# Kernel optimization log

Measured on AMD Instinct MI355X. Metric: run time of the kernel, lower is better.

## Reference

```python
import jax, jax.numpy as jnp
import numpy as np

# Neuron / sim params from init_kwargs
THETA = 1.0        # thr
TAU_RHO = 0.5      # grad_width (surrogate width, used only in backward)
SCALE_RHO = 1.0    # grad_scale
NUM_TS = 100


def avg_pool4(x):
    # SLAYER pool(4): conv3d with constant weight 1/16 over 4x4 spatial, stride 4 == average pool
    N, C, H, W, T = x.shape
    return x.reshape(N, C, H // 4, 4, W // 4, 4, T).mean(axis=(3, 5))


def conv7(x, w):
    # torch Conv3d over (H, W, T) with kernel (7,7,1), padding (3,3,0), stride 1, no bias
    return jax.lax.conv_general_dilated(
        x, w, window_strides=(1, 1, 1),
        padding=((3, 3), (3, 3), (0, 0)),
        dimension_numbers=('NCHWT', 'OIHWT', 'NCHWT'))


def psp(x):
    # IAF synaptic kernel = Heaviside step => psp is cumulative sum over time (Ts = 1)
    return jnp.cumsum(x, axis=-1)


def spike_scan(p):
    # Integrate-and-fire spike generation with reset-by-subtraction (scaleRef=1):
    # v[t] = psp[t] - theta * (#spikes before t); spike when v[t] >= theta.
    p_t = jnp.moveaxis(p, -1, 0)  # [T, N, C, H, W]
    count0 = jnp.zeros(p.shape[:-1], p.dtype)

    def step(count, pt):
        v = pt - THETA * count
        s = (v >= THETA).astype(pt.dtype)
        return count + s, (s, v)

    _, (s, v) = jax.lax.scan(step, count0, p_t)
    return jnp.moveaxis(s, 0, -1), jnp.moveaxis(v, 0, -1)


def setup_inputs() -> dict:
    key = jax.random.key(0)
    k0, k1, k2, k3 = jax.random.split(key, 4)
    data = jax.random.uniform(k0, (8, 2, 256, 256, NUM_TS), dtype=jnp.float32)
    # learned parameters (bias=False in SLAYER conv/dense)
    w_conv0 = jax.random.normal(k1, (4, 2, 7, 7, 1), dtype=jnp.float32) * 0.2
    w_conv1 = jax.random.normal(k2, (8, 4, 7, 7, 1), dtype=jnp.float32) * 0.2
    w_dense = jax.random.normal(k3, (2, 8, 4, 4, 1), dtype=jnp.float32) * 0.2
    return {"data": data, "w_conv0": w_conv0, "w_conv1": w_conv1, "w_dense": w_dense}


def reference(data, w_conv0, w_conv1, w_dense):
    x = conv7(avg_pool4(data), w_conv0)     # [8,4,64,64,T]
    s0, _ = spike_scan(psp(x))
    x = conv7(avg_pool4(s0), w_conv1)       # [8,8,16,16,T]
    s1, _ = spike_scan(psp(x))
    x = avg_pool4(s1)                       # [8,8,4,4,T]
    # dense((4,4,8) -> 2): conv3d whose kernel spans the full spatial extent
    out = jnp.einsum('nchwt,ochw->not', x, w_dense[..., 0])  # [8,2,T]
    return out
```

## Files before the change

### kernel.cpp

```cpp
#include <hip/hip_runtime.h>
#include <hip/hip_bf16.h>
#include <stdint.h>


#define T_ 100

__global__ __launch_bounds__(256) void k1_pool0(const float* __restrict__ in,
                                                double* __restrict__ out) {
    __shared__ double lds[64 * 101];
    int b = blockIdx.x;
    int h = b & 63, c = (b >> 6) & 1, n = b >> 7;
    const float* inb = in + ((size_t)((n * 2 + c) * 256 + 4 * h) * 256) * 100;
    for (int k = 0; k < 7; ++k) {
        int e = threadIdx.x + (k << 8);
        if (e < 1600) {
            int w = e / 25, tq = e % 25;
            double s0 = 0.0, s1 = 0.0, s2 = 0.0, s3 = 0.0;
            #pragma unroll
            for (int a = 0; a < 4; ++a) {
                #pragma unroll
                for (int bb = 0; bb < 4; ++bb) {
                    const float4 v = *reinterpret_cast<const float4*>(
                        &inb[((size_t)(a * 256 + 4 * w + bb)) * 100 + 4 * tq]);
                    s0 += (double)v.x;
                    s1 += (double)v.y;
                    s2 += (double)v.z;
                    s3 += (double)v.w;
                }
            }
            double* lp = &lds[w * 101 + 4 * tq];
            lp[0] = s0 * 0.0625;
            lp[1] = s1 * 0.0625;
            lp[2] = s2 * 0.0625;
            lp[3] = s3 * 0.0625;
        }
    }
    __syncthreads();
    double* outb = out + ((size_t)(n * 2 + c) * 100) * 4096 + h * 64;
    for (int k = 0; k < 25; ++k) {
        int oi = threadIdx.x + (k << 8);
        int t = oi >> 6, w = oi & 63;
        outb[(size_t)t * 4096 + w] = lds[w * 101 + t];
    }
}

__global__ __launch_bounds__(256, 2) void k2a_conv0(const double* __restrict__ pooled0,
                                                    const float* __restrict__ wc0,
                                                    double* __restrict__ x0) {
    __shared__ double tile[2 * 22 * 70];
    __shared__ double wlds[392];
    int b = blockIdx.x;
    int hs = b & 3;
    int t = (b >> 2) % 100;
    int n = b / 400;
    int tid = threadIdx.x;

    for (int i = tid; i < 392; i += 256) wlds[i] = (double)wc0[i];
    {
        int lane = tid & 63, wv = tid >> 6;
        for (int r = wv; r < 44; r += 4) {
            int ci = (r >= 22) ? 1 : 0;
            int row = r - ci * 22;
            int habs = hs * 16 + row - 3;
            const double* src =
                &pooled0[((size_t)((n * 2 + ci) * 100 + t)) * 4096 + habs * 64];
            double* dst = &tile[(ci * 22 + row) * 70];
            int wabs = lane - 3;
            bool hok = (unsigned)habs < 64u;
            dst[lane] = (hok && (unsigned)wabs < 64u) ? src[wabs] : 0.0;
            if (lane < 6) {
                int wabs2 = lane + 61;
                dst[lane + 64] = (hok && (unsigned)wabs2 < 64u) ? src[wabs2] : 0.0;
            }
        }
    }
    __syncthreads();

    int w = tid & 63, hq = tid >> 6;
    int hl0 = hq * 4;
    double acc[4][4];
    #pragma unroll
    for (int co = 0; co < 4; ++co)
        #pragma unroll
        for (int j = 0; j < 4; ++j) acc[co][j] = 0.0;

    for (int ci = 0; ci < 2; ++ci) {
        #pragma unroll
        for (int kh = 0; kh < 7; ++kh) {
            const double* wp = &wlds[ci * 49 + kh * 7];
            #pragma unroll
            for (int j = 0; j < 4; ++j) {
                const double* r = &tile[(ci * 22 + hl0 + kh + j) * 70 + w];
                double v0 = r[0], v1 = r[1], v2 = r[2], v3 = r[3];
                double v4 = r[4], v5 = r[5], v6 = r[6];
                #pragma unroll
                for (int co = 0; co < 4; ++co) {
                    acc[co][j] += v0 * wp[co * 98 + 0];
                    acc[co][j] += v1 * wp[co * 98 + 1];
                    acc[co][j] += v2 * wp[co * 98 + 2];
                    acc[co][j] += v3 * wp[co * 98 + 3];
                    acc[co][j] += v4 * wp[co * 98 + 4];
                    acc[co][j] += v5 * wp[co * 98 + 5];
                    acc[co][j] += v6 * wp[co * 98 + 6];
                }
            }
        }
    }
    #pragma unroll
    for (int co = 0; co < 4; ++co)
        #pragma unroll
        for (int j = 0; j < 4; ++j)
            x0[(((size_t)(n * 4 + co) * 64 + (hs * 16 + hl0 + j)) * 100 + t) * 64 + w] =
                acc[co][j];
}

__global__ __launch_bounds__(256) void k2b_scan0_pool(const double* __restrict__ x0,
                                                      float* __restrict__ pooled1) {
    __shared__ uint8_t lsp[10][256];
    int bid = blockIdx.x;
    int g = bid >> 4, hp = bid & 15;
    int tid = threadIdx.x;
    int r = tid >> 6, w = tid & 63;
    size_t base = ((size_t)(g * 64 + hp * 4 + r) * 100) * 64 + w;
    double p = 0.0;
    int cnt = 0;
    for (int tc = 0; tc < 10; ++tc) {
        double v[10];
        #pragma unroll
        for (int j = 0; j < 10; ++j)
            v[j] = x0[base + (size_t)(tc * 10 + j) * 64];
        #pragma unroll
        for (int j = 0; j < 10; ++j) {
            p += v[j];
            int sp = (p - (double)cnt) >= 1.0;
            cnt += sp;
            lsp[j][tid] = (uint8_t)sp;
        }
        __syncthreads();
        if (tid < 160) {
            int t = tid >> 4, wp = tid & 15;
            int isum = 0;
            #pragma unroll
            for (int rr = 0; rr < 4; ++rr) {
                uint32_t u = *reinterpret_cast<const uint32_t*>(&lsp[t][rr * 64 + 4 * wp]);
                isum += (int)(u & 0xffu) + (int)((u >> 8) & 0xffu) +
                        (int)((u >> 16) & 0xffu) + (int)(u >> 24);
            }
            pooled1[((size_t)g * 100 + tc * 10 + t) * 256 + hp * 16 + wp] =
                (float)isum * 0.0625f;
        }
        __syncthreads();
    }
}

#define TC2 5
__global__ __launch_bounds__(128) void k2_conv0_scan(const double* __restrict__ pooled0,
                                                     const float* __restrict__ wc0,
                                                     uint8_t* __restrict__ s0) {
    __shared__ double tile[2 * 7 * TC2 * 70];
    int b = blockIdx.x;
    int h = b & 63, n = b >> 6;
    int tid = threadIdx.x;
    int w = tid & 63, cog = tid >> 6;
    int co0 = 2 * cog, co1 = co0 + 1;
    for (int i = tid; i < 2 * 7 * TC2 * 70; i += 128) tile[i] = 0.0;
    double p0 = 0.0, p1 = 0.0;
    int c0 = 0, c1 = 0;
    for (int ch = 0; ch < T_ / TC2; ++ch) {
        int t0 = ch * TC2;
        __syncthreads();
        for (int k = 0; k < 35; ++k) {
            int e = tid + (k << 7);
            int ww = e & 63, rowid = e >> 6;
            int ci = rowid / 35, rem = rowid % 35;
            int tt = rem / 7, r = rem % 7;
            int habs = h - 3 + r;
            if ((unsigned)habs < 64u)
                tile[((ci * 7 + r) * TC2 + tt) * 70 + ww + 3] =
                    pooled0[((size_t)((n * 2 + ci) * 100 + t0 + tt)) * 4096 + habs * 64 + ww];
        }
        __syncthreads();
        double acc0[TC2], acc1[TC2];
        #pragma unroll
        for (int tt = 0; tt < TC2; ++tt) { acc0[tt] = 0.0; acc1[tt] = 0.0; }
        for (int ci = 0; ci < 2; ++ci) {
            for (int kh = 0; kh < 7; ++kh) {
                const double* trow = &tile[((ci * 7 + kh) * TC2) * 70];
                const float* wr0 = &wc0[co0 * 98 + ci * 49 + kh * 7];
                const float* wr1 = &wc0[co1 * 98 + ci * 49 + kh * 7];
                #pragma unroll
                for (int kw = 0; kw < 7; ++kw) {
                    double wa = (double)wr0[kw];
                    double wb = (double)wr1[kw];
                    #pragma unroll
                    for (int tt = 0; tt < TC2; ++tt) {
                        double v = trow[tt * 70 + w + kw];
                        acc0[tt] += v * wa;
                        acc1[tt] += v * wb;
                    }
                }
            }
        }
        #pragma unroll
        for (int tt = 0; tt < TC2; ++tt) {
            size_t ob = ((size_t)((n * 4 + co0) * 100 + t0 + tt)) * 4096 + h * 64 + w;
            p0 += acc0[tt];
            int sp0 = (p0 - (double)c0) >= 1.0;
            c0 += sp0;
            s0[ob] = (uint8_t)sp0;
            size_t ob1 = ((size_t)((n * 4 + co1) * 100 + t0 + tt)) * 4096 + h * 64 + w;
            p1 += acc1[tt];
            int sp1 = (p1 - (double)c1) >= 1.0;
            c1 += sp1;
            s0[ob1] = (uint8_t)sp1;
        }
    }
}

__global__ __launch_bounds__(256) void k3_pool1(const uint8_t* __restrict__ s0,
                                                float* __restrict__ pooled1) {
    int oi = blockIdx.x * 256 + threadIdx.x;
    int w = oi & 15, h = (oi >> 4) & 15;
    int tc = oi >> 8;
    int t = tc % 100, nc = tc / 100;
    const uint8_t* base = s0 + ((size_t)nc * 100 + t) * 4096;
    int isum = 0;
    #pragma unroll
    for (int a = 0; a < 4; ++a) {
        uint32_t v = *reinterpret_cast<const uint32_t*>(&base[(4 * h + a) * 64 + 4 * w]);
        isum += (int)(v & 0xffu) + (int)((v >> 8) & 0xffu) +
                (int)((v >> 16) & 0xffu) + (int)(v >> 24);
    }
    pooled1[oi] = (float)isum * 0.0625f;
}

__global__ __launch_bounds__(256) void k4a_conv1(const float* __restrict__ pooled1,
                                                 const float* __restrict__ wc1,
                                                 double* __restrict__ x1) {
    __shared__ float tile[4 * 22 * 24];
    __shared__ float wl[1568];
    int b = blockIdx.x;
    int n = b / 100, t = b % 100;
    int tid = threadIdx.x;
    for (int i = tid; i < 4 * 22 * 24; i += 256) tile[i] = 0.0f;
    for (int i = tid; i < 1568; i += 256) wl[i] = wc1[i];
    __syncthreads();
    for (int k = 0; k < 4; ++k) {
        int e = tid + (k << 8);
        int w = e & 15, rowid = e >> 4;
        int ci = rowid >> 4, hr3 = rowid & 15;
        tile[(ci * 22 + hr3 + 3) * 24 + 3 + w] =
            pooled1[((size_t)((n * 4 + ci) * 100 + t)) * 256 + hr3 * 16 + w];
    }
    __syncthreads();
    int h = tid >> 4, w = tid & 15;
    double acc[8];
    #pragma unroll
    for (int co = 0; co < 8; ++co) acc[co] = 0.0;
    for (int ci = 0; ci < 4; ++ci) {
        for (int kh = 0; kh < 7; ++kh) {
            const float* trow = &tile[(ci * 22 + h + kh) * 24];
            const float* wr = &wl[ci * 49 + kh * 7];
            #pragma unroll
            for (int kw = 0; kw < 7; ++kw) {
                double v = (double)trow[w + kw];
                #pragma unroll
                for (int co = 0; co < 8; ++co)
                    acc[co] += v * (double)wr[co * 196 + kw];
            }
        }
    }
    #pragma unroll
    for (int co = 0; co < 8; ++co)
        x1[(((size_t)(n * 8 + co) * 4 + (tid >> 6)) * 100 + t) * 64 + (tid & 63)] =
            acc[co];
}

__global__ __launch_bounds__(64) void k4b_scan1(const double* __restrict__ x1,
                                                uint8_t* __restrict__ s1) {
    int bid = blockIdx.x;
    int g8 = bid >> 2, q = bid & 3;
    size_t rbase = ((size_t)(g8 * 4 + q) * 100) * 64 + threadIdx.x;
    size_t wbase = (size_t)g8 * 100 * 256 + (q << 6) + threadIdx.x;
    double p = 0.0;
    int cnt = 0;
    for (int tc = 0; tc < 10; ++tc) {
        double v[10];
        #pragma unroll
        for (int j = 0; j < 10; ++j)
            v[j] = x1[rbase + (size_t)(tc * 10 + j) * 64];
        #pragma unroll
        for (int j = 0; j < 10; ++j) {
            p += v[j];
            int sp = (p - (double)cnt) >= 1.0;
            cnt += sp;
            s1[wbase + (size_t)(tc * 10 + j) * 256] = (uint8_t)sp;
        }
    }
}

__global__ __launch_bounds__(256) void k5_dense(const uint8_t* __restrict__ s1,
                                                const float* __restrict__ wd,
                                                float* __restrict__ out) {
    __shared__ float red[2][4];
    int b = blockIdx.x;
    int n = b / 100, t = b % 100;
    int tid = threadIdx.x;
    int c = tid >> 5, H = (tid >> 1) & 15, Wg = tid & 1;
    const uint8_t* sb = s1 + ((size_t)((n * 8 + c) * 100 + t)) * 256 + H * 16 + Wg * 8;
    float sumA = 0.f, sumB = 0.f;
    #pragma unroll
    for (int j = 0; j < 4; ++j) sumA += (float)sb[j];
    #pragma unroll
    for (int j = 4; j < 8; ++j) sumB += (float)sb[j];
    int wb = c * 16 + (H >> 2) * 4 + Wg * 2;
    float o0 = sumA * wd[wb] + sumB * wd[wb + 1];
    float o1 = sumA * wd[128 + wb] + sumB * wd[128 + wb + 1];
    #pragma unroll
    for (int off = 32; off > 0; off >>= 1) {
        o0 += __shfl_down(o0, off, 64);
        o1 += __shfl_down(o1, off, 64);
    }
    int lane = tid & 63, wid = tid >> 6;
    if (lane == 0) { red[0][wid] = o0; red[1][wid] = o1; }
    __syncthreads();
    if (tid == 0) {
        float a = (red[0][0] + red[0][1]) + (red[0][2] + red[0][3]);
        float bsum = (red[1][0] + red[1][1]) + (red[1][2] + red[1][3]);
        out[(size_t)(n * 2) * 100 + t] = a * 0.0625f;
        out[(size_t)(n * 2 + 1) * 100 + t] = bsum * 0.0625f;
    }
}

extern "C" void kernel_launch(void* const* d_in, const int* in_sizes, int n_in,
                              void* d_out, int out_size, void* d_ws, size_t ws_size,
                              hipStream_t stream) {
    const float* data = (const float*)d_in[0];
    const float* w0   = (const float*)d_in[1];
    const float* w1   = (const float*)d_in[2];
    const float* wd   = (const float*)d_in[3];
    float* out = (float*)d_out;
    char* ws = (char*)d_ws;

    const size_t NEED_SPLIT = 157286400;

    if (ws_size >= NEED_SPLIT) {
        double*  pooled0 = (double*)(ws);
        double*  x0      = (double*)(ws + 52428800);
        float*   pooled1 = (float*)(ws);
        double*  x1      = (double*)(ws + 4194304);
        uint8_t* s1      = (uint8_t*)(ws + 25165824);

        k1_pool0<<<1024, 256, 0, stream>>>(data, pooled0);
        k2a_conv0<<<3200, 256, 0, stream>>>(pooled0, w0, x0);
        k2b_scan0_pool<<<512, 256, 0, stream>>>(x0, pooled1);
        k4a_conv1<<<800, 256, 0, stream>>>(pooled1, w1, x1);
        k4b_scan1<<<256, 64, 0, stream>>>(x1, s1);
        k5_dense<<<800, 256, 0, stream>>>(s1, wd, out);
    } else {
        double*  pooled0 = (double*)(ws);
        uint8_t* s0      = (uint8_t*)(ws + 52428800);
        float*   pooled1 = (float*)(ws + 65536000);
        double*  x1      = (double*)(ws + 68812800);
        uint8_t* s1      = (uint8_t*)(ws + 85196800);

        k1_pool0<<<1024, 256, 0, stream>>>(data, pooled0);
        k2_conv0_scan<<<512, 128, 0, stream>>>(pooled0, w0, s0);
        k3_pool1<<<3200, 256, 0, stream>>>(s0, pooled1);
        k4a_conv1<<<800, 256, 0, stream>>>(pooled1, w1, x1);
        k4b_scan1<<<256, 64, 0, stream>>>(x1, s1);
        k5_dense<<<800, 256, 0, stream>>>(s1, wd, out);
    }
}
```

Baseline: 235.9 us.

## Use sliding register windows for conv0 and conv1 with 4 rows per thread

The conv0 inner loop now keeps a 4x7 window of input rows in registers and shifts it down one row per kernel-row step, loading each tile row once instead of once per kernel row. Weights are loaded once per output channel and reused across four output rows. conv1 gets the same treatment: each thread now computes 4 output rows, the block shrinks from 256 to 64 threads, and the zero-fill plus interior-load double pass is replaced by one padded load. This cuts LDS traffic, at the cost of more registers per thread, 32 double accumulators in conv1, and fewer threads per block for conv1.

```diff
diff --git a/kernel.cpp b/kernel.cpp
--- a/kernel.cpp
+++ b/kernel.cpp
@@ -84,25 +84,42 @@
         #pragma unroll
         for (int j = 0; j < 4; ++j) acc[co][j] = 0.0;
 
+    double win[4][7];
     for (int ci = 0; ci < 2; ++ci) {
+        #pragma unroll
+        for (int j = 0; j < 4; ++j) {
+            const double* rp = &tile[(ci * 22 + hl0 + j) * 70 + w];
+            #pragma unroll
+            for (int k = 0; k < 7; ++k) win[j][k] = rp[k];
+        }
         #pragma unroll
         for (int kh = 0; kh < 7; ++kh) {
             const double* wp = &wlds[ci * 49 + kh * 7];
             #pragma unroll
-            for (int j = 0; j < 4; ++j) {
-                const double* r = &tile[(ci * 22 + hl0 + kh + j) * 70 + w];
-                double v0 = r[0], v1 = r[1], v2 = r[2], v3 = r[3];
-                double v4 = r[4], v5 = r[5], v6 = r[6];
-                #pragma unroll
-                for (int co = 0; co < 4; ++co) {
-                    acc[co][j] += v0 * wp[co * 98 + 0];
-                    acc[co][j] += v1 * wp[co * 98 + 1];
-                    acc[co][j] += v2 * wp[co * 98 + 2];
-                    acc[co][j] += v3 * wp[co * 98 + 3];
-                    acc[co][j] += v4 * wp[co * 98 + 4];
-                    acc[co][j] += v5 * wp[co * 98 + 5];
-                    acc[co][j] += v6 * wp[co * 98 + 6];
+            for (int co = 0; co < 4; ++co) {
+                double w0 = wp[co * 98 + 0], w1 = wp[co * 98 + 1];
+                double w2 = wp[co * 98 + 2], w3 = wp[co * 98 + 3];
+                double w4 = wp[co * 98 + 4], w5 = wp[co * 98 + 5];
+                double w6 = wp[co * 98 + 6];
+                #pragma unroll
+                for (int j = 0; j < 4; ++j) {
+                    acc[co][j] += win[j][0] * w0;
+                    acc[co][j] += win[j][1] * w1;
+                    acc[co][j] += win[j][2] * w2;
+                    acc[co][j] += win[j][3] * w3;
+                    acc[co][j] += win[j][4] * w4;
+                    acc[co][j] += win[j][5] * w5;
+                    acc[co][j] += win[j][6] * w6;
                 }
+            }
+            if (kh < 6) {
+                #pragma unroll
+                for (int j = 0; j < 3; ++j)
+                    #pragma unroll
+                    for (int k = 0; k < 7; ++k) win[j][k] = win[j + 1][k];
+                const double* rp = &tile[(ci * 22 + hl0 + kh + 4) * 70 + w];
+                #pragma unroll
+                for (int k = 0; k < 7; ++k) win[3][k] = rp[k];
             }
         }
     }
@@ -234,46 +251,80 @@
     pooled1[oi] = (float)isum * 0.0625f;
 }
 
-__global__ __launch_bounds__(256) void k4a_conv1(const float* __restrict__ pooled1,
-                                                 const float* __restrict__ wc1,
-                                                 double* __restrict__ x1) {
+__global__ __launch_bounds__(64) void k4a_conv1(const float* __restrict__ pooled1,
+                                                const float* __restrict__ wc1,
+                                                double* __restrict__ x1) {
     __shared__ float tile[4 * 22 * 24];
     __shared__ float wl[1568];
     int b = blockIdx.x;
     int n = b / 100, t = b % 100;
     int tid = threadIdx.x;
-    for (int i = tid; i < 4 * 22 * 24; i += 256) tile[i] = 0.0f;
-    for (int i = tid; i < 1568; i += 256) wl[i] = wc1[i];
+    for (int i = tid; i < 1568; i += 64) wl[i] = wc1[i];
+    for (int i = tid; i < 2112; i += 64) {
+        int ci = i / 528, rem = i % 528;
+        int r = rem / 24, c = rem % 24;
+        int habs = r - 3, wabs = c - 3;
+        float v = 0.f;
+        if ((unsigned)habs < 16u && (unsigned)wabs < 16u)
+            v = pooled1[((size_t)((n * 4 + ci) * 100 + t)) * 256 + habs * 16 + wabs];
+        tile[i] = v;
+    }
     __syncthreads();
-    for (int k = 0; k < 4; ++k) {
-        int e = tid + (k << 8);
-        int w = e & 15, rowid = e >> 4;
-        int ci = rowid >> 4, hr3 = rowid & 15;
-        tile[(ci * 22 + hr3 + 3) * 24 + 3 + w] =
-            pooled1[((size_t)((n * 4 + ci) * 100 + t)) * 256 + hr3 * 16 + w];
-    }
-    __syncthreads();
-    int h = tid >> 4, w = tid & 15;
-    double acc[8];
-    #pragma unroll
-    for (int co = 0; co < 8; ++co) acc[co] = 0.0;
+    int w = tid & 15, hq = tid >> 4;
+    int hl0 = hq * 4;
+    double acc[8][4];
+    #pragma unroll
+    for (int co = 0; co < 8; ++co)
+        #pragma unroll
+        for (int j = 0; j < 4; ++j) acc[co][j] = 0.0;
+
+    float win[4][7];
     for (int ci = 0; ci < 4; ++ci) {
+        #pragma unroll
+        for (int j = 0; j < 4; ++j) {
+            const float* rp = &tile[(ci * 22 + hl0 + j) * 24 + w];
+            #pragma unroll
+            for (int k = 0; k < 7; ++k) win[j][k] = rp[k];
+        }
+        #pragma unroll
         for (int kh = 0; kh < 7; ++kh) {
-            const float* trow = &tile[(ci * 22 + h + kh) * 24];
             const float* wr = &wl[ci * 49 + kh * 7];
             #pragma unroll
-            for (int kw = 0; kw < 7; ++kw) {
-                double v = (double)trow[w + kw];
-                #pragma unroll
-                for (int co = 0; co < 8; ++co)
-                    acc[co] += v * (double)wr[co * 196 + kw];
+            for (int co = 0; co < 8; ++co) {
+                double w0 = (double)wr[co * 196 + 0], w1 = (double)wr[co * 196 + 1];
+                double w2 = (double)wr[co * 196 + 2], w3 = (double)wr[co * 196 + 3];
+                double w4 = (double)wr[co * 196 + 4], w5 = (double)wr[co * 196 + 5];
+                double w6 = (double)wr[co * 196 + 6];
+                #pragma unroll
+                for (int j = 0; j < 4; ++j) {
+                    acc[co][j] += (double)win[j][0] * w0;
+                    acc[co][j] += (double)win[j][1] * w1;
+                    acc[co][j] += (double)win[j][2] * w2;
+                    acc[co][j] += (double)win[j][3] * w3;
+                    acc[co][j] += (double)win[j][4] * w4;
+                    acc[co][j] += (double)win[j][5] * w5;
+                    acc[co][j] += (double)win[j][6] * w6;
+                }
+            }
+            if (kh < 6) {
+                #pragma unroll
+                for (int j = 0; j < 3; ++j)
+                    #pragma unroll
+                    for (int k = 0; k < 7; ++k) win[j][k] = win[j + 1][k];
+                const float* rp = &tile[(ci * 22 + hl0 + kh + 4) * 24 + w];
+                #pragma unroll
+                for (int k = 0; k < 7; ++k) win[3][k] = rp[k];
             }
         }
     }
     #pragma unroll
     for (int co = 0; co < 8; ++co)
-        x1[(((size_t)(n * 8 + co) * 4 + (tid >> 6)) * 100 + t) * 64 + (tid & 63)] =
-            acc[co];
+        #pragma unroll
+        for (int j = 0; j < 4; ++j) {
+            int hw = (hl0 + j) * 16 + w;
+            x1[(((size_t)(n * 8 + co) * 4 + (hw >> 6)) * 100 + t) * 64 + (hw & 63)] =
+                acc[co][j];
+        }
 }
 
 __global__ __launch_bounds__(64) void k4b_scan1(const double* __restrict__ x1,
@@ -354,7 +405,7 @@
         k1_pool0<<<1024, 256, 0, stream>>>(data, pooled0);
         k2a_conv0<<<3200, 256, 0, stream>>>(pooled0, w0, x0);
         k2b_scan0_pool<<<512, 256, 0, stream>>>(x0, pooled1);
-        k4a_conv1<<<800, 256, 0, stream>>>(pooled1, w1, x1);
+        k4a_conv1<<<800, 64, 0, stream>>>(pooled1, w1, x1);
         k4b_scan1<<<256, 64, 0, stream>>>(x1, s1);
         k5_dense<<<800, 256, 0, stream>>>(s1, wd, out);
     } else {
@@ -367,7 +418,7 @@
         k1_pool0<<<1024, 256, 0, stream>>>(data, pooled0);
         k2_conv0_scan<<<512, 128, 0, stream>>>(pooled0, w0, s0);
         k3_pool1<<<3200, 256, 0, stream>>>(s0, pooled1);
-        k4a_conv1<<<800, 256, 0, stream>>>(pooled1, w1, x1);
+        k4a_conv1<<<800, 64, 0, stream>>>(pooled1, w1, x1);
         k4b_scan1<<<256, 64, 0, stream>>>(x1, s1);
         k5_dense<<<800, 256, 0, stream>>>(s1, wd, out);
     }
```

New measurement: 247.0 us. 1.05x slower.
